# Kernel optimization log

Hardware: AMD Instinct MI355X
Metric: run time of the kernel (lower is better)

Reference implementation:

```python
import jax, jax.numpy as jnp
import numpy as np

B, S, D = 4, 2048, 768
H = 12
HD = D // H  # 64


def setup_inputs() -> dict:
    key = jax.random.key(0)
    k1, k2, k3 = jax.random.split(key, 3)
    scale_qkv = (6.0 / (D + 3 * D)) ** 0.5  # xavier_uniform bound
    scale_o = (6.0 / (D + D)) ** 0.5
    return {
        "x": jax.random.normal(k1, (B, S, D), dtype=jnp.float32),
        "w_qkv": jax.random.uniform(k2, (3 * D, D), dtype=jnp.float32, minval=-scale_qkv, maxval=scale_qkv),
        "b_qkv": jnp.zeros((3 * D,), dtype=jnp.float32),
        "w_o": jax.random.uniform(k3, (D, D), dtype=jnp.float32, minval=-scale_o, maxval=scale_o),
        "b_o": jnp.zeros((D,), dtype=jnp.float32),
    }


def reference(x, w_qkv, b_qkv, w_o, b_o):
    b, s, _ = x.shape
    # qkv projection: [B,S,3D]
    qkv = jnp.einsum("bsd,ed->bse", x, w_qkv) + b_qkv
    # [B,S,H,3*HD] -> [B,H,S,3*HD]
    qkv = qkv.reshape(b, s, H, 3 * HD).transpose(0, 2, 1, 3)
    q, k, v = jnp.split(qkv, 3, axis=-1)  # each [B,H,S,HD]
    # scaled dot-product attention (full score matrix, as in source)
    attn_logits = jnp.einsum("bhqd,bhkd->bhqk", q, k) / np.sqrt(HD).astype(np.float32)
    attention = jax.nn.softmax(attn_logits, axis=-1)
    values = jnp.einsum("bhqk,bhkd->bhqd", attention, v)
    # merge heads: [B,S,D]
    values = values.transpose(0, 2, 1, 3).reshape(b, s, D)
    out = jnp.einsum("bsd,ed->bse", values, w_o) + b_o
    return out
```

## Files before the change

### kernel.cpp

```cpp
#include <hip/hip_runtime.h>
#include <hip/hip_bf16.h>

#define BB 4
#define SS 2048
#define DD 768
#define HH 12
#define HDD 64
#define QKVW 2304

typedef _Float16 h8 __attribute__((ext_vector_type(8)));
typedef _Float16 h2 __attribute__((ext_vector_type(2)));
typedef __fp16 fp16x2 __attribute__((ext_vector_type(2)));
typedef float f4 __attribute__((ext_vector_type(4)));
typedef unsigned int u4 __attribute__((ext_vector_type(4)));

struct __align__(8) Half4 { _Float16 x, y, z, w; };
struct __align__(8) H2x2 { h2 a, b; };

#define QSCALE 0.18033688011112042f

__device__ __forceinline__ h2 pk_cvt(float a, float b) {
    fp16x2 r = __builtin_amdgcn_cvt_pkrtz(a, b);
    return __builtin_bit_cast(h2, r);
}

__device__ __forceinline__ void pl_swap32(unsigned &a, unsigned &b) {
    asm("v_permlane32_swap_b32 %0, %1" : "+v"(a), "+v"(b));
}
__device__ __forceinline__ void pl_swap16(unsigned &a, unsigned &b) {
    asm("v_permlane16_swap_b32 %0, %1" : "+v"(a), "+v"(b));
}

#define N4_X   (BB * SS * DD / 4)
#define N4_WQ  (QKVW * DD / 4)
#define N4_WO  (DD * DD / 4)
#define N4_ALL (N4_X + N4_WQ + N4_WO)

__global__ __launch_bounds__(256) void cvt_all(const float* __restrict__ x,
                                               const float* __restrict__ wq,
                                               const float* __restrict__ wo,
                                               _Float16* __restrict__ xh,
                                               _Float16* __restrict__ wqh,
                                               _Float16* __restrict__ woh) {
    int i = blockIdx.x * 256 + threadIdx.x;
    const float* src;
    _Float16* dst;
    if (i < N4_X) {
        src = x; dst = xh;
    } else if (i < N4_X + N4_WQ) {
        i -= N4_X; src = wq; dst = wqh;
    } else {
        i -= N4_X + N4_WQ; src = wo; dst = woh;
    }
    const float4 v = ((const float4*)src)[i];
    Half4 h = {(_Float16)v.x, (_Float16)v.y, (_Float16)v.z, (_Float16)v.w};
    ((Half4*)dst)[i] = h;
}

__device__ __forceinline__ void gload16(const _Float16* g, _Float16* l) {
    __builtin_amdgcn_global_load_lds(
        (const __attribute__((address_space(1))) unsigned int*)g,
        (__attribute__((address_space(3))) unsigned int*)l, 16, 0, 0);
}

template <int EPI>
__global__ __launch_bounds__(256) void gemm_f16(const _Float16* __restrict__ A,
                                                const _Float16* __restrict__ B,
                                                const float* __restrict__ bias,
                                                float* __restrict__ Cf,
                                                _Float16* __restrict__ Ch,
                                                _Float16* __restrict__ VTg,
                                                int M, int N, int K) {
    __shared__ alignas(16) _Float16 Ash[128 * 64];
    __shared__ alignas(16) _Float16 Bsh[128 * 64];

    const int tid = threadIdx.x;
    const int lane = tid & 63;
    const int w = tid >> 6;
    const int l15 = lane & 15;
    const int qd = lane >> 4;
    const int wm = w & 1;
    const int wn = w >> 1;
    const int m0 = blockIdx.y * 128;
    const int n0 = blockIdx.x * 128;
    const int ldsb = w * 512;

    f4 acc[4][4];
#pragma unroll
    for (int mt = 0; mt < 4; ++mt)
#pragma unroll
        for (int nt = 0; nt < 4; ++nt) acc[mt][nt] = (f4){0.f, 0.f, 0.f, 0.f};

    const _Float16* Ab = A + (size_t)m0 * K;
    const _Float16* Bb = B + (size_t)n0 * K;

    const int srow = tid >> 3;
    const int cg = ((tid & 7) ^ (srow & 7)) * 8;
    const int x7 = l15 & 7;

    for (int k0 = 0; k0 < K; k0 += 64) {
        __syncthreads();
#pragma unroll
        for (int i = 0; i < 4; ++i) {
            const size_t gsrc = (size_t)(i * 32 + srow) * K + k0 + cg;
            gload16(Ab + gsrc, Ash + i * 2048 + ldsb);
            gload16(Bb + gsrc, Bsh + i * 2048 + ldsb);
        }
        __syncthreads();

#pragma unroll
        for (int s = 0; s < 2; ++s) {
            h8 aF[4], bF[4];
#pragma unroll
            for (int mt = 0; mt < 4; ++mt)
                aF[mt] = *(const h8*)&Ash[(wm * 64 + mt * 16 + l15) * 64
                                          + (((s * 4 + qd) ^ x7) << 3)];
#pragma unroll
            for (int nt = 0; nt < 4; ++nt)
                bF[nt] = *(const h8*)&Bsh[(wn * 64 + nt * 16 + l15) * 64
                                          + (((s * 4 + qd) ^ x7) << 3)];
#pragma unroll
            for (int mt = 0; mt < 4; ++mt)
#pragma unroll
                for (int nt = 0; nt < 4; ++nt)
                    acc[mt][nt] = __builtin_amdgcn_mfma_f32_16x16x32_f16(
                        bF[nt], aF[mt], acc[mt][nt], 0, 0, 0);
        }
    }

#pragma unroll
    for (int mt = 0; mt < 4; ++mt) {
        const int m = m0 + wm * 64 + mt * 16 + l15;
#pragma unroll
        for (int nt = 0; nt < 4; ++nt) {
            const int nb = n0 + wn * 64 + nt * 16 + qd * 4;
            const float4 bv = *(const float4*)(bias + nb);
            f4 v = acc[mt][nt];
            v[0] += bv.x; v[1] += bv.y; v[2] += bv.z; v[3] += bv.w;
            if (EPI == 0) {
                *(float4*)(Cf + (size_t)m * N + nb) = (float4){v[0], v[1], v[2], v[3]};
            } else {
                const int typ = (nb >> 6) % 3;
                if (typ == 2) {
                    const int h_ = nb / 192;
                    const int d0 = nb - h_ * 192 - 128;
                    _Float16* vtp = VTg + ((size_t)(m >> 11) * 768 + h_ * 64 + d0) * 2048
                                    + (m & 2047);
                    vtp[0] = (_Float16)v[0];
                    vtp[2048] = (_Float16)v[1];
                    vtp[2 * 2048] = (_Float16)v[2];
                    vtp[3 * 2048] = (_Float16)v[3];
                } else {
                    if (typ == 0) {
                        v[0] *= QSCALE; v[1] *= QSCALE; v[2] *= QSCALE; v[3] *= QSCALE;
                    }
                    H2x2 pk;
                    pk.a = pk_cvt(v[0], v[1]);
                    pk.b = pk_cvt(v[2], v[3]);
                    *(H2x2*)(Ch + (size_t)m * N + nb) = pk;
                }
            }
        }
    }
}

__global__ __launch_bounds__(256, 3) void attn_mfma(const _Float16* __restrict__ qkvh,
                                                    const _Float16* __restrict__ vT,
                                                    _Float16* __restrict__ vh) {
    __shared__ alignas(16) _Float16 Kh[2][64 * 64];
    __shared__ alignas(16) _Float16 VTs[2][64 * 64];

    const int tid = threadIdx.x;
    const int lane = tid & 63;
    const int w = tid >> 6;
    const int l15 = lane & 15;
    const int qd = lane >> 4;
    const int h = blockIdx.y;
    const int b = blockIdx.z;
    const int qbase = blockIdx.x * 128 + w * 32;

    const size_t bhrow = (size_t)b * SS;
    const int hcol = h * 192;
    const int x7 = l15 & 7;

    h8 bQ[2][2];
#pragma unroll
    for (int nt = 0; nt < 2; ++nt)
#pragma unroll
        for (int kc = 0; kc < 2; ++kc)
            bQ[nt][kc] = *(const h8*)(qkvh + (bhrow + qbase + nt * 16 + l15) * QKVW
                                      + hcol + kc * 32 + qd * 8);

    f4 O[4][2];
#pragma unroll
    for (int dt = 0; dt < 4; ++dt)
#pragma unroll
        for (int nt = 0; nt < 2; ++nt) O[dt][nt] = (f4){0.f, 0.f, 0.f, 0.f};
    f4 lacc[2] = {(f4){0.f, 0.f, 0.f, 0.f}, (f4){0.f, 0.f, 0.f, 0.f}};

    h8 ones;
#pragma unroll
    for (int i = 0; i < 8; ++i) ones[i] = (_Float16)1.0f;

    const int srow = tid >> 3;
    const int cgx = ((tid & 7) ^ (srow & 7)) << 3;
    const _Float16* kgbase = qkvh + bhrow * QKVW + hcol + 64 + cgx;
    const _Float16* vgbase = vT + ((size_t)b * 768 + h * 64) * 2048 + cgx;
    const int ldso = w * 512;

    auto stage = [&](int kt, int buf) {
#pragma unroll
        for (int i = 0; i < 2; ++i) {
            gload16(kgbase + (size_t)(kt * 64 + i * 32 + srow) * QKVW,
                    &Kh[buf][i * 2048 + ldso]);
            gload16(vgbase + (size_t)(i * 32 + srow) * 2048 + kt * 64,
                    &VTs[buf][i * 2048 + ldso]);
        }
    };

    stage(0, 0);

    for (int kt = 0; kt < SS / 64; ++kt) {
        const int buf = kt & 1;
        __syncthreads();
        if (kt + 1 < SS / 64) stage(kt + 1, buf ^ 1);

        h8 aK[4][2];
#pragma unroll
        for (int mt = 0; mt < 4; ++mt)
#pragma unroll
            for (int kc = 0; kc < 2; ++kc)
                aK[mt][kc] = *(const h8*)&Kh[buf][(mt * 16 + l15) * 64
                                                  + (((kc * 4 + qd) ^ x7) << 3)];

        h8 bP[2][2];
#pragma unroll
        for (int nt = 0; nt < 2; ++nt) {
            unsigned c[4][2];
#pragma unroll
            for (int mt = 0; mt < 4; ++mt) {
                f4 z = (f4){0.f, 0.f, 0.f, 0.f};
                z = __builtin_amdgcn_mfma_f32_16x16x32_f16(aK[mt][0], bQ[nt][0], z, 0, 0, 0);
                z = __builtin_amdgcn_mfma_f32_16x16x32_f16(aK[mt][1], bQ[nt][1], z, 0, 0, 0);
                c[mt][0] = __builtin_bit_cast(unsigned, pk_cvt(exp2f(z[0]), exp2f(z[1])));
                c[mt][1] = __builtin_bit_cast(unsigned, pk_cvt(exp2f(z[2]), exp2f(z[3])));
            }
#pragma unroll
            for (int kc = 0; kc < 2; ++kc) {
                unsigned x0 = c[2 * kc][0], y0 = c[2 * kc + 1][0];
                pl_swap32(x0, y0);
                pl_swap16(x0, y0);
                unsigned x1 = c[2 * kc][1], y1 = c[2 * kc + 1][1];
                pl_swap32(x1, y1);
                pl_swap16(x1, y1);
                u4 t = (u4){x0, x1, y0, y1};
                bP[nt][kc] = __builtin_bit_cast(h8, t);
            }
        }

#pragma unroll
        for (int nt = 0; nt < 2; ++nt) {
            lacc[nt] = __builtin_amdgcn_mfma_f32_16x16x32_f16(ones, bP[nt][0], lacc[nt], 0, 0, 0);
            lacc[nt] = __builtin_amdgcn_mfma_f32_16x16x32_f16(ones, bP[nt][1], lacc[nt], 0, 0, 0);
        }

        h8 aV[4][2];
#pragma unroll
        for (int dt = 0; dt < 4; ++dt)
#pragma unroll
            for (int kc = 0; kc < 2; ++kc)
                aV[dt][kc] = *(const h8*)&VTs[buf][(dt * 16 + l15) * 64
                                                   + (((kc * 4 + qd) ^ x7) << 3)];
#pragma unroll
        for (int dt = 0; dt < 4; ++dt)
#pragma unroll
            for (int nt = 0; nt < 2; ++nt) {
                O[dt][nt] = __builtin_amdgcn_mfma_f32_16x16x32_f16(aV[dt][0], bP[nt][0], O[dt][nt], 0, 0, 0);
                O[dt][nt] = __builtin_amdgcn_mfma_f32_16x16x32_f16(aV[dt][1], bP[nt][1], O[dt][nt], 0, 0, 0);
            }
    }

#pragma unroll
    for (int nt = 0; nt < 2; ++nt) {
        const float linv = 1.0f / lacc[nt][0];
        const size_t row = bhrow + qbase + nt * 16 + l15;
#pragma unroll
        for (int dt = 0; dt < 4; ++dt) {
            f4 o = O[dt][nt];
            Half4 oh;
            oh.x = (_Float16)(o[0] * linv);
            oh.y = (_Float16)(o[1] * linv);
            oh.z = (_Float16)(o[2] * linv);
            oh.w = (_Float16)(o[3] * linv);
            *(Half4*)(vh + row * DD + h * 64 + dt * 16 + qd * 4) = oh;
        }
    }
}

extern "C" void kernel_launch(void* const* d_in, const int* in_sizes, int n_in,
                              void* d_out, int out_size, void* d_ws, size_t ws_size,
                              hipStream_t stream) {
    const float* x     = (const float*)d_in[0];
    const float* w_qkv = (const float*)d_in[1];
    const float* b_qkv = (const float*)d_in[2];
    const float* w_o   = (const float*)d_in[3];
    const float* b_o   = (const float*)d_in[4];
    float* out = (float*)d_out;

    const int M = BB * SS;

    _Float16* p = (_Float16*)d_ws;
    _Float16* qkv_h = p;  p += (size_t)M * QKVW;
    _Float16* vT = p;     p += (size_t)BB * DD * SS;
    _Float16* xh = p;     p += (size_t)M * DD;
    _Float16* vh = p;     p += (size_t)M * DD;
    _Float16* wqh = p;    p += (size_t)QKVW * DD;
    _Float16* woh = p;    p += (size_t)DD * DD;

    cvt_all<<<N4_ALL / 256, 256, 0, stream>>>(x, w_qkv, w_o, xh, wqh, woh);

    gemm_f16<1><<<dim3(QKVW / 128, M / 128), 256, 0, stream>>>(
        xh, wqh, b_qkv, nullptr, qkv_h, vT, M, QKVW, DD);

    attn_mfma<<<dim3(SS / 128, HH, BB), 256, 0, stream>>>(qkv_h, vT, vh);

    gemm_f16<0><<<dim3(DD / 128, M / 128), 256, 0, stream>>>(
        vh, woh, b_o, out, nullptr, nullptr, M, DD, DD);
}
```

Before: 245.9 us.

## Split attention block into 8 waves of 16 query rows with setprio and native exp2

The attention kernel now uses 512 threads per block, with each wave owning 16 query rows instead of 32. This halves per-wave register state (Q fragments, O accumulators, P tiles) and lets all 512 threads share the K/V staging with one load each per tile. It also replaces exp2f with the native amdgcn exp2 builtin and wraps MFMA sections in s_setprio to favour matrix issue across waves. In exchange, each K/V tile loaded into LDS is reused by more waves but with less work per wave, and every wave still reads the full K/V fragments from LDS, so LDS read traffic per query row doubles.

```diff
diff --git a/kernel.cpp b/kernel.cpp
--- a/kernel.cpp
+++ b/kernel.cpp
@@ -22,6 +22,10 @@
 __device__ __forceinline__ h2 pk_cvt(float a, float b) {
     fp16x2 r = __builtin_amdgcn_cvt_pkrtz(a, b);
     return __builtin_bit_cast(h2, r);
+}
+
+__device__ __forceinline__ float fexp2(float x) {
+    return __builtin_amdgcn_exp2f(x);
 }
 
 __device__ __forceinline__ void pl_swap32(unsigned &a, unsigned &b) {
@@ -164,7 +168,7 @@
     }
 }
 
-__global__ __launch_bounds__(256, 3) void attn_mfma(const _Float16* __restrict__ qkvh,
+__global__ __launch_bounds__(512, 6) void attn_mfma(const _Float16* __restrict__ qkvh,
                                                     const _Float16* __restrict__ vT,
                                                     _Float16* __restrict__ vh) {
     __shared__ alignas(16) _Float16 Kh[2][64 * 64];
@@ -177,45 +181,36 @@
     const int qd = lane >> 4;
     const int h = blockIdx.y;
     const int b = blockIdx.z;
-    const int qbase = blockIdx.x * 128 + w * 32;
+    const int qrow = blockIdx.x * 128 + w * 16;
 
     const size_t bhrow = (size_t)b * SS;
     const int hcol = h * 192;
     const int x7 = l15 & 7;
 
-    h8 bQ[2][2];
-#pragma unroll
-    for (int nt = 0; nt < 2; ++nt)
-#pragma unroll
-        for (int kc = 0; kc < 2; ++kc)
-            bQ[nt][kc] = *(const h8*)(qkvh + (bhrow + qbase + nt * 16 + l15) * QKVW
-                                      + hcol + kc * 32 + qd * 8);
-
-    f4 O[4][2];
-#pragma unroll
-    for (int dt = 0; dt < 4; ++dt)
-#pragma unroll
-        for (int nt = 0; nt < 2; ++nt) O[dt][nt] = (f4){0.f, 0.f, 0.f, 0.f};
-    f4 lacc[2] = {(f4){0.f, 0.f, 0.f, 0.f}, (f4){0.f, 0.f, 0.f, 0.f}};
+    h8 bQ[2];
+#pragma unroll
+    for (int kc = 0; kc < 2; ++kc)
+        bQ[kc] = *(const h8*)(qkvh + (bhrow + qrow + l15) * QKVW
+                              + hcol + kc * 32 + qd * 8);
+
+    f4 O[4];
+#pragma unroll
+    for (int dt = 0; dt < 4; ++dt) O[dt] = (f4){0.f, 0.f, 0.f, 0.f};
+    f4 lacc = (f4){0.f, 0.f, 0.f, 0.f};
 
     h8 ones;
 #pragma unroll
     for (int i = 0; i < 8; ++i) ones[i] = (_Float16)1.0f;
 
-    const int srow = tid >> 3;
-    const int cgx = ((tid & 7) ^ (srow & 7)) << 3;
-    const _Float16* kgbase = qkvh + bhrow * QKVW + hcol + 64 + cgx;
-    const _Float16* vgbase = vT + ((size_t)b * 768 + h * 64) * 2048 + cgx;
+    const int trow = (tid >> 3) & 63;
+    const int cgx = ((tid & 7) ^ (trow & 7)) << 3;
+    const _Float16* kgbase = qkvh + (bhrow + trow) * QKVW + hcol + 64 + cgx;
+    const _Float16* vgbase = vT + ((size_t)b * 768 + h * 64 + trow) * 2048 + cgx;
     const int ldso = w * 512;
 
     auto stage = [&](int kt, int buf) {
-#pragma unroll
-        for (int i = 0; i < 2; ++i) {
-            gload16(kgbase + (size_t)(kt * 64 + i * 32 + srow) * QKVW,
-                    &Kh[buf][i * 2048 + ldso]);
-            gload16(vgbase + (size_t)(i * 32 + srow) * 2048 + kt * 64,
-                    &VTs[buf][i * 2048 + ldso]);
-        }
+        gload16(kgbase + (size_t)kt * 64 * QKVW, &Kh[buf][ldso]);
+        gload16(vgbase + kt * 64, &VTs[buf][ldso]);
     };
 
     stage(0, 0);
@@ -233,35 +228,29 @@
                 aK[mt][kc] = *(const h8*)&Kh[buf][(mt * 16 + l15) * 64
                                                   + (((kc * 4 + qd) ^ x7) << 3)];
 
-        h8 bP[2][2];
-#pragma unroll
-        for (int nt = 0; nt < 2; ++nt) {
-            unsigned c[4][2];
-#pragma unroll
-            for (int mt = 0; mt < 4; ++mt) {
-                f4 z = (f4){0.f, 0.f, 0.f, 0.f};
-                z = __builtin_amdgcn_mfma_f32_16x16x32_f16(aK[mt][0], bQ[nt][0], z, 0, 0, 0);
-                z = __builtin_amdgcn_mfma_f32_16x16x32_f16(aK[mt][1], bQ[nt][1], z, 0, 0, 0);
-                c[mt][0] = __builtin_bit_cast(unsigned, pk_cvt(exp2f(z[0]), exp2f(z[1])));
-                c[mt][1] = __builtin_bit_cast(unsigned, pk_cvt(exp2f(z[2]), exp2f(z[3])));
-            }
-#pragma unroll
-            for (int kc = 0; kc < 2; ++kc) {
-                unsigned x0 = c[2 * kc][0], y0 = c[2 * kc + 1][0];
-                pl_swap32(x0, y0);
-                pl_swap16(x0, y0);
-                unsigned x1 = c[2 * kc][1], y1 = c[2 * kc + 1][1];
-                pl_swap32(x1, y1);
-                pl_swap16(x1, y1);
-                u4 t = (u4){x0, x1, y0, y1};
-                bP[nt][kc] = __builtin_bit_cast(h8, t);
-            }
-        }
-
-#pragma unroll
-        for (int nt = 0; nt < 2; ++nt) {
-            lacc[nt] = __builtin_amdgcn_mfma_f32_16x16x32_f16(ones, bP[nt][0], lacc[nt], 0, 0, 0);
-            lacc[nt] = __builtin_amdgcn_mfma_f32_16x16x32_f16(ones, bP[nt][1], lacc[nt], 0, 0, 0);
+        unsigned c[4][2];
+        __builtin_amdgcn_s_setprio(1);
+#pragma unroll
+        for (int mt = 0; mt < 4; ++mt) {
+            f4 z = (f4){0.f, 0.f, 0.f, 0.f};
+            z = __builtin_amdgcn_mfma_f32_16x16x32_f16(aK[mt][0], bQ[0], z, 0, 0, 0);
+            z = __builtin_amdgcn_mfma_f32_16x16x32_f16(aK[mt][1], bQ[1], z, 0, 0, 0);
+            c[mt][0] = __builtin_bit_cast(unsigned, pk_cvt(fexp2(z[0]), fexp2(z[1])));
+            c[mt][1] = __builtin_bit_cast(unsigned, pk_cvt(fexp2(z[2]), fexp2(z[3])));
+        }
+        __builtin_amdgcn_s_setprio(0);
+
+        h8 bP[2];
+#pragma unroll
+        for (int kc = 0; kc < 2; ++kc) {
+            unsigned x0 = c[2 * kc][0], y0 = c[2 * kc + 1][0];
+            pl_swap32(x0, y0);
+            pl_swap16(x0, y0);
+            unsigned x1 = c[2 * kc][1], y1 = c[2 * kc + 1][1];
+            pl_swap32(x1, y1);
+            pl_swap16(x1, y1);
+            u4 t = (u4){x0, x1, y0, y1};
+            bP[kc] = __builtin_bit_cast(h8, t);
         }
 
         h8 aV[4][2];
@@ -271,29 +260,29 @@
             for (int kc = 0; kc < 2; ++kc)
                 aV[dt][kc] = *(const h8*)&VTs[buf][(dt * 16 + l15) * 64
                                                    + (((kc * 4 + qd) ^ x7) << 3)];
-#pragma unroll
-        for (int dt = 0; dt < 4; ++dt)
-#pragma unroll
-            for (int nt = 0; nt < 2; ++nt) {
-                O[dt][nt] = __builtin_amdgcn_mfma_f32_16x16x32_f16(aV[dt][0], bP[nt][0], O[dt][nt], 0, 0, 0);
-                O[dt][nt] = __builtin_amdgcn_mfma_f32_16x16x32_f16(aV[dt][1], bP[nt][1], O[dt][nt], 0, 0, 0);
-            }
-    }
-
-#pragma unroll
-    for (int nt = 0; nt < 2; ++nt) {
-        const float linv = 1.0f / lacc[nt][0];
-        const size_t row = bhrow + qbase + nt * 16 + l15;
+
+        __builtin_amdgcn_s_setprio(1);
+        lacc = __builtin_amdgcn_mfma_f32_16x16x32_f16(ones, bP[0], lacc, 0, 0, 0);
+        lacc = __builtin_amdgcn_mfma_f32_16x16x32_f16(ones, bP[1], lacc, 0, 0, 0);
 #pragma unroll
         for (int dt = 0; dt < 4; ++dt) {
-            f4 o = O[dt][nt];
-            Half4 oh;
-            oh.x = (_Float16)(o[0] * linv);
-            oh.y = (_Float16)(o[1] * linv);
-            oh.z = (_Float16)(o[2] * linv);
-            oh.w = (_Float16)(o[3] * linv);
-            *(Half4*)(vh + row * DD + h * 64 + dt * 16 + qd * 4) = oh;
-        }
+            O[dt] = __builtin_amdgcn_mfma_f32_16x16x32_f16(aV[dt][0], bP[0], O[dt], 0, 0, 0);
+            O[dt] = __builtin_amdgcn_mfma_f32_16x16x32_f16(aV[dt][1], bP[1], O[dt], 0, 0, 0);
+        }
+        __builtin_amdgcn_s_setprio(0);
+    }
+
+    const float linv = 1.0f / lacc[0];
+    const size_t row = bhrow + qrow + l15;
+#pragma unroll
+    for (int dt = 0; dt < 4; ++dt) {
+        f4 o = O[dt];
+        Half4 oh;
+        oh.x = (_Float16)(o[0] * linv);
+        oh.y = (_Float16)(o[1] * linv);
+        oh.z = (_Float16)(o[2] * linv);
+        oh.w = (_Float16)(o[3] * linv);
+        *(Half4*)(vh + row * DD + h * 64 + dt * 16 + qd * 4) = oh;
     }
 }
 
@@ -322,7 +311,7 @@
     gemm_f16<1><<<dim3(QKVW / 128, M / 128), 256, 0, stream>>>(
         xh, wqh, b_qkv, nullptr, qkv_h, vT, M, QKVW, DD);
 
-    attn_mfma<<<dim3(SS / 128, HH, BB), 256, 0, stream>>>(qkv_h, vT, vh);
+    attn_mfma<<<dim3(SS / 128, HH, BB), 512, 0, stream>>>(qkv_h, vT, vh);
 
     gemm_f16<0><<<dim3(DD / 128, M / 128), 256, 0, stream>>>(
         vh, woh, b_o, out, nullptr, nullptr, M, DD, DD);
```

Measured after the change: 224.8 us. 8.6% less time.
